# Performance work log

Measured on AMD Instinct MI355X. Metric: run time of the kernel, lower is better.

Reference implementation:

```python
import jax, jax.numpy as jnp
import numpy as np


def grad_G(x):
    # x: [B,1,H,W] -> [B,2,H,W]; forward finite differences, circular padding
    dx = jnp.roll(x, -1, axis=-2) - x  # diff along H
    dy = jnp.roll(x, -1, axis=-1) - x  # diff along W
    return jnp.concatenate([dx, dy], axis=1)


def grad_GH(q):
    # adjoint of grad_G: [B,2,H,W] -> [B,1,H,W]  (= -div with circular BC)
    qx = q[:, 0:1]
    qy = q[:, 1:2]
    return (jnp.roll(qx, 1, axis=-2) - qx) + (jnp.roll(qy, 1, axis=-1) - qy)


def setup_inputs() -> dict:
    key = jax.random.key(0)
    k1, k2 = jax.random.split(key)
    B, H, W = 4, 512, 512
    x = jax.random.normal(k1, (B, 1, H, W), dtype=jnp.float32)
    lambda_map = jax.random.uniform(k2, (B, 2, H, W), dtype=jnp.float32)
    return {
        "x": x,
        "lambda_map": lambda_map,
        "tau": jnp.float32(10.0),
        "sigma": jnp.float32(10.0),
        "theta": jnp.float32(10.0),
        "T": 128,
    }


def reference(x, lambda_map, tau, sigma, theta, T):
    # operator norms: ||A^H A|| = 1, ||G^H G|| = 12  ->  L = sqrt(13)
    L = jnp.sqrt(jnp.asarray(13.0, x.dtype))
    sig = jax.nn.sigmoid(sigma) / L
    ta = jax.nn.sigmoid(tau) / L
    th = jax.nn.sigmoid(theta)
    xnoisy = x

    def step(carry, _):
        x0, xbar, p, q = carry
        # dual update for data term
        p = (p + sig * (xbar - xnoisy)) / (1.0 + sig)
        # dual update for TV term: project onto [-lambda, lambda] per component
        q = jnp.clip(q + sig * grad_G(xbar), -lambda_map, lambda_map)
        # primal update
        x1 = x0 - ta * p - ta * grad_GH(q)
        # over-relaxation (extra update on the last step is dead code, as in torch)
        xbar = x1 + th * (x1 - x0)
        return (x1, xbar, p, q), None

    B, _, H, W = x.shape
    q0 = jnp.zeros((B, 2, H, W), dtype=x.dtype)
    (x1, _, _, _), _ = jax.lax.scan(step, (x, x, x, q0), None, length=T)
    return x1
```

## Files before the change

### kernel.cpp

```cpp
#include <hip/hip_runtime.h>


#define B_ 4
#define H_ 512
#define W_ 512
#define R_ 8
#define NBANDS_ (H_ / R_)
#define NB_ (B_ * NBANDS_)
#define T_ 128
#define PAD_ 32

__device__ __forceinline__ float clampl(float v, float l) {
    return fminf(fmaxf(v, -l), l);
}

#define P2ROW(r, QXU)                                                        \
  {                                                                          \
    const float qyl_ = QY[2 * sub + (r)][jl];                                \
    _Pragma("unroll")                                                        \
    for (int k = 0; k < 4; ++k) {                                            \
      float left = k ? qyn[r][k - 1] : qyl_;                                 \
      float dv = ((QXU)[k] - qxn[r][k]) + (left - qyn[r][k]);                \
      float x1 = x0_[r][k] - ta * pn[r][k] - ta * dv;                        \
      xbn[r][k] = x1 + th * (x1 - x0_[r][k]);                                \
      x0_[r][k] = x1;                                                        \
      p_[r][k]  = pn[r][k];                                                  \
      qx_[r][k] = qxn[r][k];                                                 \
      qy_[r][k] = qyn[r][k];                                                 \
    }                                                                        \
    *(float4*)&XB[2 * sub + (r) + 1][j0] =                                   \
        make_float4(xbn[r][0], xbn[r][1], xbn[r][2], xbn[r][3]);             \
  }

#define PUBLISH(ROWARR, BUF, FLAG)                                           \
  {                                                                          \
    unsigned long long lo_, hi_;                                             \
    __builtin_memcpy(&lo_, &(ROWARR)[0], 8);                                 \
    __builtin_memcpy(&hi_, &(ROWARR)[2], 8);                                 \
    unsigned long long* dst_ =                                               \
        (unsigned long long*)&(BUF)[(size_t)bb * W_ + j0];                   \
    __hip_atomic_store(dst_, lo_, __ATOMIC_RELAXED,                          \
                       __HIP_MEMORY_SCOPE_AGENT);                            \
    __hip_atomic_store(dst_ + 1, hi_, __ATOMIC_RELAXED,                      \
                       __HIP_MEMORY_SCOPE_AGENT);                            \
    asm volatile("s_waitcnt vmcnt(0)" ::: "memory");                         \
    if ((tid & 63) == 0)                                                     \
      __hip_atomic_store(&(FLAG)[bb * PAD_ + widx], t + 1,                   \
                         __ATOMIC_RELAXED, __HIP_MEMORY_SCOPE_AGENT);        \
  }

__global__ __launch_bounds__(512, 2) void pdnn_persistent(
    const float* __restrict__ x, const float* __restrict__ lam,
    const float* __restrict__ tau_p, const float* __restrict__ sigma_p,
    const float* __restrict__ theta_p, float* __restrict__ out,
    float* __restrict__ topA, float* __restrict__ botA,
    float* __restrict__ topB, float* __restrict__ botB,
    int* __restrict__ topflag, int* __restrict__ botflag)
{
    __shared__ float XB[R_ + 2][W_];
    __shared__ float QXS[3][W_];
    __shared__ float QY[R_][W_];

    const int tid  = threadIdx.x;
    const int c    = tid & 127;
    const int sub  = tid >> 7;
    const int widx = (tid >> 6) & 1;
    const int bb   = blockIdx.x;
    const int b    = bb >> 6;
    const int lb   = bb & 63;
    const int r0   = lb * R_;
    const int j0   = c * 4;

    const size_t plane = (size_t)H_ * W_;
    const float* ximg  = x   + (size_t)b * plane;
    const float* l0img = lam + (size_t)b * 2 * plane;
    const float* l1img = l0img + plane;
    float*       oimg  = out + (size_t)b * plane;

    const float Linv = 0.27735009811261457f;
    const float sg  = Linv / (1.f + __expf(-sigma_p[0]));
    const float ta  = Linv / (1.f + __expf(-tau_p[0]));
    const float th  = 1.f  / (1.f + __expf(-theta_p[0]));
    const float i1s = 1.f / (1.f + sg);

    for (int k = sub; k < R_ + 2; k += 4) {
        int rw = r0 - 1 + k;
        rw = (rw < 0) ? rw + H_ : (rw >= H_ ? rw - H_ : rw);
        *(float4*)&XB[k][j0] = *(const float4*)&ximg[(size_t)rw * W_ + j0];
    }
    float l0h_[4] = {0.f, 0.f, 0.f, 0.f};
    if (sub == 0) {
        int rm1 = r0 ? r0 - 1 : H_ - 1;
        float4 a = *(const float4*)&l0img[(size_t)rm1 * W_ + j0];
        l0h_[0]=a.x; l0h_[1]=a.y; l0h_[2]=a.z; l0h_[3]=a.w;
    }

    const int ra = r0 + 2 * sub;
    float p_[2][4], x0_[2][4], xn_[2][4], l0_[2][4], l1_[2][4], qx_[2][4], qy_[2][4];
    #pragma unroll
    for (int r = 0; r < 2; ++r) {
        const size_t ro = (size_t)(ra + r) * W_ + j0;
        float4 v  = *(const float4*)&ximg[ro];
        float4 a0 = *(const float4*)&l0img[ro];
        float4 a1 = *(const float4*)&l1img[ro];
        p_[r][0]=v.x;  p_[r][1]=v.y;  p_[r][2]=v.z;  p_[r][3]=v.w;
        x0_[r][0]=v.x; x0_[r][1]=v.y; x0_[r][2]=v.z; x0_[r][3]=v.w;
        xn_[r][0]=v.x; xn_[r][1]=v.y; xn_[r][2]=v.z; xn_[r][3]=v.w;
        l0_[r][0]=a0.x; l0_[r][1]=a0.y; l0_[r][2]=a0.z; l0_[r][3]=a0.w;
        l1_[r][0]=a1.x; l1_[r][1]=a1.y; l1_[r][2]=a1.z; l1_[r][3]=a1.w;
        #pragma unroll
        for (int k = 0; k < 4; ++k) { qx_[r][k] = 0.f; qy_[r][k] = 0.f; }
    }
    float qxh[4] = {0.f, 0.f, 0.f, 0.f};

    const int above = (b << 6) | (lb ? lb - 1 : NBANDS_ - 1);
    const int below = (b << 6) | (lb == NBANDS_ - 1 ? 0 : lb + 1);
    const int jr = (j0 + 4) & (W_ - 1);
    const int jl = (j0 + W_ - 1) & (W_ - 1);

    __syncthreads();

    for (int t = 0; t < T_; ++t) {
        float hx[4];
        if (sub == 0) {
            if (t == 0) {
                hx[0] = XB[0][j0]; hx[1] = XB[0][j0 + 1];
                hx[2] = XB[0][j0 + 2]; hx[3] = XB[0][j0 + 3];
            } else {
                const float* botr = (t & 1) ? botB : botA;
                while (__hip_atomic_load(&botflag[above * PAD_ + widx],
                                         __ATOMIC_RELAXED, __HIP_MEMORY_SCOPE_AGENT) < t) {}
                asm volatile("" ::: "memory");
                const unsigned long long* src =
                    (const unsigned long long*)&botr[(size_t)above * W_ + j0];
                unsigned long long lo = __hip_atomic_load(src,     __ATOMIC_RELAXED, __HIP_MEMORY_SCOPE_AGENT);
                unsigned long long hi = __hip_atomic_load(src + 1, __ATOMIC_RELAXED, __HIP_MEMORY_SCOPE_AGENT);
                __builtin_memcpy(&hx[0], &lo, 8);
                __builtin_memcpy(&hx[2], &hi, 8);
            }
        } else if (sub == 3) {
            if (t == 0) {
                hx[0] = XB[R_ + 1][j0]; hx[1] = XB[R_ + 1][j0 + 1];
                hx[2] = XB[R_ + 1][j0 + 2]; hx[3] = XB[R_ + 1][j0 + 3];
            } else {
                const float* topr = (t & 1) ? topB : topA;
                while (__hip_atomic_load(&topflag[below * PAD_ + widx],
                                         __ATOMIC_RELAXED, __HIP_MEMORY_SCOPE_AGENT) < t) {}
                asm volatile("" ::: "memory");
                const unsigned long long* src =
                    (const unsigned long long*)&topr[(size_t)below * W_ + j0];
                unsigned long long lo = __hip_atomic_load(src,     __ATOMIC_RELAXED, __HIP_MEMORY_SCOPE_AGENT);
                unsigned long long hi = __hip_atomic_load(src + 1, __ATOMIC_RELAXED, __HIP_MEMORY_SCOPE_AGENT);
                __builtin_memcpy(&hx[0], &lo, 8);
                __builtin_memcpy(&hx[2], &hi, 8);
            }
        }

        float qxn[2][4], qyn[2][4], pn[2][4], xcs[4];
        #pragma unroll
        for (int r = 0; r < 2; ++r) {
            const int li = 2 * sub + r + 1;
            float xc[4], xd[4];
            #pragma unroll
            for (int k = 0; k < 4; ++k) { xc[k] = XB[li][j0 + k]; xd[k] = XB[li + 1][j0 + k]; }
            float xcr = XB[li][jr];
            if (r == 0 && sub == 0) {
                xcs[0] = xc[0]; xcs[1] = xc[1]; xcs[2] = xc[2]; xcs[3] = xc[3];
            }
            if (r == 1 && sub == 3) {
                xcs[0] = xc[0]; xcs[1] = xc[1]; xcs[2] = xc[2]; xcs[3] = xc[3];
            }
            #pragma unroll
            for (int k = 0; k < 4; ++k) {
                float right = (k < 3) ? xc[k + 1] : xcr;
                if (!(r == 1 && sub == 3))
                    qxn[r][k] = clampl(qx_[r][k] + sg * (xd[k] - xc[k]), l0_[r][k]);
                qyn[r][k] = clampl(qy_[r][k] + sg * (right - xc[k]), l1_[r][k]);
                pn[r][k]  = (p_[r][k] + sg * (xc[k] - xn_[r][k])) * i1s;
            }
            *(float4*)&QY[2 * sub + r][j0] = make_float4(qyn[r][0], qyn[r][1], qyn[r][2], qyn[r][3]);
        }
        if (sub < 3)
            *(float4*)&QXS[sub][j0] = make_float4(qxn[1][0], qxn[1][1], qxn[1][2], qxn[1][3]);

        float qxhn[4];
        if (sub == 0) {
            #pragma unroll
            for (int k = 0; k < 4; ++k)
                qxhn[k] = clampl(qxh[k] + sg * (xcs[k] - hx[k]), l0h_[k]);
        }
        if (sub == 3) {
            #pragma unroll
            for (int k = 0; k < 4; ++k)
                qxn[1][k] = clampl(qx_[1][k] + sg * (hx[k] - xcs[k]), l0_[1][k]);
        }
        __syncthreads();

        float xbn[2][4];
        const bool pub = (t < T_ - 1);
        float* topw = ((t + 1) & 1) ? topB : topA;
        float* botw = ((t + 1) & 1) ? botB : botA;
        if (sub == 3) {
            P2ROW(1, qxn[0]);
            if (pub) PUBLISH(xbn[1], botw, botflag);
            float qxs[4];
            { float4 qq = *(const float4*)&QXS[2][j0];
              qxs[0]=qq.x; qxs[1]=qq.y; qxs[2]=qq.z; qxs[3]=qq.w; }
            P2ROW(0, qxs);
        } else if (sub == 0) {
            P2ROW(0, qxhn);
            if (pub) PUBLISH(xbn[0], topw, topflag);
            P2ROW(1, qxn[0]);
            #pragma unroll
            for (int k = 0; k < 4; ++k) qxh[k] = qxhn[k];
        } else {
            float qxs[4];
            { float4 qq = *(const float4*)&QXS[sub - 1][j0];
              qxs[0]=qq.x; qxs[1]=qq.y; qxs[2]=qq.z; qxs[3]=qq.w; }
            P2ROW(0, qxs);
            P2ROW(1, qxn[0]);
        }

        if (!pub) {
            #pragma unroll
            for (int r = 0; r < 2; ++r)
                *(float4*)&oimg[(size_t)(ra + r) * W_ + j0] =
                    make_float4(x0_[r][0], x0_[r][1], x0_[r][2], x0_[r][3]);
        }
        __syncthreads();
    }
}

extern "C" void kernel_launch(void* const* d_in, const int* in_sizes, int n_in,
                              void* d_out, int out_size, void* d_ws, size_t ws_size,
                              hipStream_t stream) {
    const float* x       = (const float*)d_in[0];
    const float* lam     = (const float*)d_in[1];
    const float* tau_p   = (const float*)d_in[2];
    const float* sigma_p = (const float*)d_in[3];
    const float* theta_p = (const float*)d_in[4];

    float* out = (float*)d_out;
    float* ws  = (float*)d_ws;
    const size_t HALO = (size_t)NB_ * W_;
    float* topA = ws + 0 * HALO;
    float* botA = ws + 1 * HALO;
    float* topB = ws + 2 * HALO;
    float* botB = ws + 3 * HALO;
    int*   topflag = (int*)(ws + 4 * HALO);
    int*   botflag = topflag + NB_ * PAD_;

    (void)hipMemsetAsync(topflag, 0, 2 * NB_ * PAD_ * sizeof(int), stream);

    pdnn_persistent<<<dim3(NB_), dim3(512), 0, stream>>>(
        x, lam, tau_p, sigma_p, theta_p, out,
        topA, botA, topB, botB, topflag, botflag);
}
```

Measured before the change: 251.4 us.

## Tag halo values with step counter to replace flag-based inter-block sync

Each published halo float is packed with its timestep tag into a 64-bit word, so consumers can validate the data directly instead of polling a separate flag after a store fence. This removes the producer's s_waitcnt vmcnt(0) wait and the flag round trip. The initial halo read becomes a non-blocking attempt issued before local dual updates, with spinning deferred until after them, which overlaps communication with compute. The cost is twice the halo traffic and a larger workspace memset.

```diff
diff --git a/kernel.cpp b/kernel.cpp
--- a/kernel.cpp
+++ b/kernel.cpp
@@ -8,10 +8,31 @@
 #define NBANDS_ (H_ / R_)
 #define NB_ (B_ * NBANDS_)
 #define T_ 128
-#define PAD_ 32
 
 __device__ __forceinline__ float clampl(float v, float l) {
     return fminf(fmaxf(v, -l), l);
+}
+
+__device__ __forceinline__ unsigned long long packft(float f, unsigned tag) {
+    union { float f; unsigned u; } cv; cv.f = f;
+    return ((unsigned long long)tag << 32) | (unsigned long long)cv.u;
+}
+
+__device__ __forceinline__ bool try_halo(const unsigned long long* src,
+                                         unsigned want, float* hv) {
+    unsigned long long a0 = __hip_atomic_load(src + 0, __ATOMIC_RELAXED, __HIP_MEMORY_SCOPE_AGENT);
+    unsigned long long a1 = __hip_atomic_load(src + 1, __ATOMIC_RELAXED, __HIP_MEMORY_SCOPE_AGENT);
+    unsigned long long a2 = __hip_atomic_load(src + 2, __ATOMIC_RELAXED, __HIP_MEMORY_SCOPE_AGENT);
+    unsigned long long a3 = __hip_atomic_load(src + 3, __ATOMIC_RELAXED, __HIP_MEMORY_SCOPE_AGENT);
+    if (((unsigned)(a0 >> 32) != want) | ((unsigned)(a1 >> 32) != want) |
+        ((unsigned)(a2 >> 32) != want) | ((unsigned)(a3 >> 32) != want))
+        return false;
+    union { unsigned u; float f; } cv;
+    cv.u = (unsigned)a0; hv[0] = cv.f;
+    cv.u = (unsigned)a1; hv[1] = cv.f;
+    cv.u = (unsigned)a2; hv[2] = cv.f;
+    cv.u = (unsigned)a3; hv[3] = cv.f;
+    return true;
 }
 
 #define P2ROW(r, QXU)                                                        \
@@ -32,30 +53,25 @@
         make_float4(xbn[r][0], xbn[r][1], xbn[r][2], xbn[r][3]);             \
   }
 
-#define PUBLISH(ROWARR, BUF, FLAG)                                           \
+#define PUBLISH(ROWARR, BUF)                                                 \
   {                                                                          \
-    unsigned long long lo_, hi_;                                             \
-    __builtin_memcpy(&lo_, &(ROWARR)[0], 8);                                 \
-    __builtin_memcpy(&hi_, &(ROWARR)[2], 8);                                 \
-    unsigned long long* dst_ =                                               \
-        (unsigned long long*)&(BUF)[(size_t)bb * W_ + j0];                   \
-    __hip_atomic_store(dst_, lo_, __ATOMIC_RELAXED,                          \
-                       __HIP_MEMORY_SCOPE_AGENT);                            \
-    __hip_atomic_store(dst_ + 1, hi_, __ATOMIC_RELAXED,                      \
-                       __HIP_MEMORY_SCOPE_AGENT);                            \
-    asm volatile("s_waitcnt vmcnt(0)" ::: "memory");                         \
-    if ((tid & 63) == 0)                                                     \
-      __hip_atomic_store(&(FLAG)[bb * PAD_ + widx], t + 1,                   \
-                         __ATOMIC_RELAXED, __HIP_MEMORY_SCOPE_AGENT);        \
+    unsigned long long* dst_ = (BUF) + ((((size_t)bb << 7) | c) << 2);       \
+    __hip_atomic_store(dst_ + 0, packft((ROWARR)[0], (unsigned)(t + 1)),     \
+                       __ATOMIC_RELAXED, __HIP_MEMORY_SCOPE_AGENT);          \
+    __hip_atomic_store(dst_ + 1, packft((ROWARR)[1], (unsigned)(t + 1)),     \
+                       __ATOMIC_RELAXED, __HIP_MEMORY_SCOPE_AGENT);          \
+    __hip_atomic_store(dst_ + 2, packft((ROWARR)[2], (unsigned)(t + 1)),     \
+                       __ATOMIC_RELAXED, __HIP_MEMORY_SCOPE_AGENT);          \
+    __hip_atomic_store(dst_ + 3, packft((ROWARR)[3], (unsigned)(t + 1)),     \
+                       __ATOMIC_RELAXED, __HIP_MEMORY_SCOPE_AGENT);          \
   }
 
 __global__ __launch_bounds__(512, 2) void pdnn_persistent(
     const float* __restrict__ x, const float* __restrict__ lam,
     const float* __restrict__ tau_p, const float* __restrict__ sigma_p,
     const float* __restrict__ theta_p, float* __restrict__ out,
-    float* __restrict__ topA, float* __restrict__ botA,
-    float* __restrict__ topB, float* __restrict__ botB,
-    int* __restrict__ topflag, int* __restrict__ botflag)
+    unsigned long long* __restrict__ topA, unsigned long long* __restrict__ botA,
+    unsigned long long* __restrict__ topB, unsigned long long* __restrict__ botB)
 {
     __shared__ float XB[R_ + 2][W_];
     __shared__ float QXS[3][W_];
@@ -64,7 +80,6 @@
     const int tid  = threadIdx.x;
     const int c    = tid & 127;
     const int sub  = tid >> 7;
-    const int widx = (tid >> 6) & 1;
     const int bb   = blockIdx.x;
     const int b    = bb >> 6;
     const int lb   = bb & 63;
@@ -122,37 +137,26 @@
 
     for (int t = 0; t < T_; ++t) {
         float hx[4];
+        bool got = true;
+        const unsigned long long* hsrc = nullptr;
+        const unsigned want = (unsigned)t;
         if (sub == 0) {
             if (t == 0) {
                 hx[0] = XB[0][j0]; hx[1] = XB[0][j0 + 1];
                 hx[2] = XB[0][j0 + 2]; hx[3] = XB[0][j0 + 3];
             } else {
-                const float* botr = (t & 1) ? botB : botA;
-                while (__hip_atomic_load(&botflag[above * PAD_ + widx],
-                                         __ATOMIC_RELAXED, __HIP_MEMORY_SCOPE_AGENT) < t) {}
-                asm volatile("" ::: "memory");
-                const unsigned long long* src =
-                    (const unsigned long long*)&botr[(size_t)above * W_ + j0];
-                unsigned long long lo = __hip_atomic_load(src,     __ATOMIC_RELAXED, __HIP_MEMORY_SCOPE_AGENT);
-                unsigned long long hi = __hip_atomic_load(src + 1, __ATOMIC_RELAXED, __HIP_MEMORY_SCOPE_AGENT);
-                __builtin_memcpy(&hx[0], &lo, 8);
-                __builtin_memcpy(&hx[2], &hi, 8);
+                const unsigned long long* botr = (t & 1) ? botB : botA;
+                hsrc = botr + ((((size_t)above << 7) | c) << 2);
+                got = try_halo(hsrc, want, hx);
             }
         } else if (sub == 3) {
             if (t == 0) {
                 hx[0] = XB[R_ + 1][j0]; hx[1] = XB[R_ + 1][j0 + 1];
                 hx[2] = XB[R_ + 1][j0 + 2]; hx[3] = XB[R_ + 1][j0 + 3];
             } else {
-                const float* topr = (t & 1) ? topB : topA;
-                while (__hip_atomic_load(&topflag[below * PAD_ + widx],
-                                         __ATOMIC_RELAXED, __HIP_MEMORY_SCOPE_AGENT) < t) {}
-                asm volatile("" ::: "memory");
-                const unsigned long long* src =
-                    (const unsigned long long*)&topr[(size_t)below * W_ + j0];
-                unsigned long long lo = __hip_atomic_load(src,     __ATOMIC_RELAXED, __HIP_MEMORY_SCOPE_AGENT);
-                unsigned long long hi = __hip_atomic_load(src + 1, __ATOMIC_RELAXED, __HIP_MEMORY_SCOPE_AGENT);
-                __builtin_memcpy(&hx[0], &lo, 8);
-                __builtin_memcpy(&hx[2], &hi, 8);
+                const unsigned long long* topr = (t & 1) ? topB : topA;
+                hsrc = topr + ((((size_t)below << 7) | c) << 2);
+                got = try_halo(hsrc, want, hx);
             }
         }
 
@@ -183,6 +187,10 @@
         if (sub < 3)
             *(float4*)&QXS[sub][j0] = make_float4(qxn[1][0], qxn[1][1], qxn[1][2], qxn[1][3]);
 
+        if (!got) {
+            do { } while (!try_halo(hsrc, want, hx));
+        }
+
         float qxhn[4];
         if (sub == 0) {
             #pragma unroll
@@ -198,18 +206,18 @@
 
         float xbn[2][4];
         const bool pub = (t < T_ - 1);
-        float* topw = ((t + 1) & 1) ? topB : topA;
-        float* botw = ((t + 1) & 1) ? botB : botA;
+        unsigned long long* topw = ((t + 1) & 1) ? topB : topA;
+        unsigned long long* botw = ((t + 1) & 1) ? botB : botA;
         if (sub == 3) {
             P2ROW(1, qxn[0]);
-            if (pub) PUBLISH(xbn[1], botw, botflag);
+            if (pub) PUBLISH(xbn[1], botw);
             float qxs[4];
             { float4 qq = *(const float4*)&QXS[2][j0];
               qxs[0]=qq.x; qxs[1]=qq.y; qxs[2]=qq.z; qxs[3]=qq.w; }
             P2ROW(0, qxs);
         } else if (sub == 0) {
             P2ROW(0, qxhn);
-            if (pub) PUBLISH(xbn[0], topw, topflag);
+            if (pub) PUBLISH(xbn[0], topw);
             P2ROW(1, qxn[0]);
             #pragma unroll
             for (int k = 0; k < 4; ++k) qxh[k] = qxhn[k];
@@ -241,18 +249,15 @@
     const float* theta_p = (const float*)d_in[4];
 
     float* out = (float*)d_out;
-    float* ws  = (float*)d_ws;
-    const size_t HALO = (size_t)NB_ * W_;
-    float* topA = ws + 0 * HALO;
-    float* botA = ws + 1 * HALO;
-    float* topB = ws + 2 * HALO;
-    float* botB = ws + 3 * HALO;
-    int*   topflag = (int*)(ws + 4 * HALO);
-    int*   botflag = topflag + NB_ * PAD_;
-
-    (void)hipMemsetAsync(topflag, 0, 2 * NB_ * PAD_ * sizeof(int), stream);
+    unsigned long long* hws = (unsigned long long*)d_ws;
+    const size_t HSLOT = (size_t)NB_ * 128 * 4;
+    unsigned long long* topA = hws + 0 * HSLOT;
+    unsigned long long* botA = hws + 1 * HSLOT;
+    unsigned long long* topB = hws + 2 * HSLOT;
+    unsigned long long* botB = hws + 3 * HSLOT;
+
+    (void)hipMemsetAsync(hws, 0, 4 * HSLOT * sizeof(unsigned long long), stream);
 
     pdnn_persistent<<<dim3(NB_), dim3(512), 0, stream>>>(
-        x, lam, tau_p, sigma_p, theta_p, out,
-        topA, botA, topB, botB, topflag, botflag);
-}
+        x, lam, tau_p, sigma_p, theta_p, out, topA, botA, topB, botB);
+}
```

Result: slower. 344.5 us (+37.0%).
